# Performance work log

Hardware: AMD Instinct MI355X
Metric: run time of the kernel (lower is better)

Reference implementation:

```python
import jax, jax.numpy as jnp
import numpy as np

B, L, DM, E, N, R, S = 2, 1024, 512, 1024, 16, 32, 64
BN_SCALE = float(1.0 / np.sqrt(1.0 + 1e-5))  # eval-mode BatchNorm1d with default running stats


def _ssm(x, Wx, bx, Wdt, bdt, A_log, D):
    # x: [B,L,E] -> Mamba selective scan output [B,L,E]
    dbc = x @ Wx.T + bx                                   # [B,L,R+2N]
    delta = jax.nn.softplus(dbc[..., :R] @ Wdt.T + bdt)   # [B,L,E]
    Bm = dbc[..., R:R + N]                                # [B,L,N]
    Cm = dbc[..., R + N:]                                 # [B,L,N]
    A = -jnp.exp(A_log)                                   # [E,N]
    dA = jnp.exp(delta[..., None] * A)                    # [B,L,E,N]
    dBx = delta[..., None] * Bm[:, :, None, :] * x[..., None]

    def comb(c1, c2):
        a1, b1 = c1
        a2, b2 = c2
        return a1 * a2, b1 * a2 + b2

    _, h = jax.lax.associative_scan(comb, (dA, dBx), axis=1)  # [B,L,E,N]
    return jnp.einsum('blen,bln->ble', h, Cm) + D * x


def _gmask_idx(length, batch):
    ref = (length + 1) // 2
    idx = jnp.arange(length, dtype=jnp.float32)
    sigma = jnp.abs(idx - ref).mean()
    w = jnp.exp(-0.5 * (idx - ref) ** 2 / sigma ** 2)
    w = w / w.sum()
    return jnp.broadcast_to(w, (batch, length))


def _gmask_vec(seq):
    length = seq.shape[1]
    ref = seq[:, (length + 1) // 2, :]
    d = jnp.linalg.norm(seq - ref[:, None, :], axis=2)    # [B,L]
    sigma = d.mean(axis=1, keepdims=True)
    w = jnp.exp(-0.5 * (d / sigma) ** 2)
    return w / w.sum(axis=1, keepdims=True)


def _spatial_attn(x, w, b):
    # x: [B,L,C]; SpatialAttention: returns weighted map in [B,C,L] layout
    xt = jnp.swapaxes(x, 1, 2)                            # [B,C,L]
    fmap = (w[0] * xt.max(axis=1) + w[1] * xt.mean(axis=1) + b) * BN_SCALE
    wmap = jax.nn.sigmoid(jax.nn.relu(fmap))[:, None, :]  # [B,1,L]
    return xt * wmap                                      # [B,C,L]


def _forward(x, W_in_x, b_in_x, W_in_z, b_in_z, convf_w, convf_b, convb_w, convb_b,
             Wx_f, bx_f, Wdt_f, bdt_f, A_log_f, D_f,
             Wx_b, bx_b, Wdt_b, bdt_b, A_log_b, D_b,
             W_cat, b_cat, sa_w, sa_b, wA_f, wV_f,
             W_proj, b_proj, W_Bi, b_Bi, tf_w, tf_b, W_out, b_out):
    b_, l_, _ = x.shape
    xi = x @ W_in_x.T + b_in_x                            # [B,L,E]
    z = x @ W_in_z.T + b_in_z                             # [B,L,E]
    # depthwise conv1d with kernel_size=1 == per-channel affine
    x_f = jax.nn.silu(xi * convf_w + convf_b)
    x_b = jax.nn.silu(jnp.flip(xi, axis=1) * convb_w + convb_b)
    y_f = jnp.tanh(_ssm(x_f, Wx_f, bx_f, Wdt_f, bdt_f, A_log_f, D_f))
    y_b = jnp.tanh(_ssm(x_b, Wx_b, bx_b, Wdt_b, bdt_b, A_log_b, D_b))
    gi = _gmask_idx(l_, b_)
    mf = jax.nn.softmax(gi * _gmask_vec(y_f), axis=1)
    mb = jax.nn.softmax(gi * _gmask_vec(y_b), axis=1)
    y_cat = jnp.concatenate([y_f * mf[..., None],
                             y_b * jnp.flip(mb[..., None], axis=1)], axis=-1)
    y = y_cat @ W_cat.T + b_cat                           # [B,L,E]
    m = jax.nn.softmax(gi * _gmask_vec(y_cat), axis=1)
    y = y * m[..., None]
    yw = _spatial_attn(y, sa_w, sa_b)                     # [B,E,L]
    y = jnp.swapaxes(yw, 1, 2)                            # [B,L,E]
    # STL tokenizer (forward direction weights)
    Aw = jax.nn.softmax(jnp.swapaxes(y @ wA_f.T, 1, 2), axis=-1)  # [B,S,L]
    u = Aw @ (y @ wV_f)                                   # [B,S,E]
    # z branch: adaptive average pool L -> S (L % S == 0), then SiLU
    zp = jax.nn.silu(jnp.swapaxes(z, 1, 2).reshape(b_, E, S, l_ // S).mean(-1))
    zt = jnp.swapaxes(zp, 1, 2)                           # [B,S,E]
    # TokenFuser -- faithful to original's .view-based memory reinterpretation
    Y = (u.reshape(b_, E, S) @ W_proj.T + b_proj).reshape(b_, S, E)
    Bw = jax.nn.sigmoid(zt @ W_Bi.T + b_Bi)               # [B,S,S]
    BwY = Bw @ Y                                          # [B,S,E]
    xj = _spatial_attn(zt, tf_w, tf_b).reshape(b_, S, E)  # view (reshape), not transpose
    out = BwY + xj
    return jnp.tanh(out @ W_out.T + b_out)                # [B,S,DM]


def setup_inputs():
    ks = jax.random.split(jax.random.key(0), 24)
    g = lambda i, shape, s=0.02: jax.random.normal(ks[i], shape, dtype=jnp.float32) * s
    A_log = jnp.log(jnp.tile(jnp.arange(1, N + 1, dtype=jnp.float32), (E, 1)))
    return dict(
        x=jax.random.normal(ks[0], (B, L, DM), dtype=jnp.float32),
        W_in_x=g(1, (E, DM)), b_in_x=jnp.zeros((E,), jnp.float32),
        W_in_z=g(2, (E, DM)), b_in_z=jnp.zeros((E,), jnp.float32),
        convf_w=1.0 + g(3, (E,)), convf_b=jnp.zeros((E,), jnp.float32),
        convb_w=1.0 + g(4, (E,)), convb_b=jnp.zeros((E,), jnp.float32),
        Wx_f=g(5, (R + 2 * N, E)), bx_f=jnp.zeros((R + 2 * N,), jnp.float32),
        Wdt_f=g(6, (E, R)), bdt_f=jnp.full((E,), -4.0, jnp.float32),
        A_log_f=A_log, D_f=jnp.ones((E,), jnp.float32),
        Wx_b=g(7, (R + 2 * N, E)), bx_b=jnp.zeros((R + 2 * N,), jnp.float32),
        Wdt_b=g(8, (E, R)), bdt_b=jnp.full((E,), -4.0, jnp.float32),
        A_log_b=A_log, D_b=jnp.ones((E,), jnp.float32),
        W_cat=g(9, (E, 2 * E)), b_cat=jnp.zeros((E,), jnp.float32),
        sa_w=g(10, (2,), 0.5), sa_b=jnp.zeros((), jnp.float32),
        wA_f=g(11, (S, E), 0.05), wV_f=g(12, (E, E), 0.02),
        W_proj=g(13, (S, S), 0.1), b_proj=jnp.zeros((S,), jnp.float32),
        W_Bi=g(14, (S, E)), b_Bi=jnp.zeros((S,), jnp.float32),
        tf_w=g(15, (2,), 0.5), tf_b=jnp.zeros((), jnp.float32),
        W_out=g(16, (DM, E)), b_out=jnp.zeros((DM,), jnp.float32),
    )


def reference(x, W_in_x, b_in_x, W_in_z, b_in_z, convf_w, convf_b, convb_w, convb_b,
              Wx_f, bx_f, Wdt_f, bdt_f, A_log_f, D_f,
              Wx_b, bx_b, Wdt_b, bdt_b, A_log_b, D_b,
              W_cat, b_cat, sa_w, sa_b, wA_f, wV_f,
              W_proj, b_proj, W_Bi, b_Bi, tf_w, tf_b, W_out, b_out):
    return _forward(x, W_in_x, b_in_x, W_in_z, b_in_z, convf_w, convf_b, convb_w, convb_b,
                    Wx_f, bx_f, Wdt_f, bdt_f, A_log_f, D_f,
                    Wx_b, bx_b, Wdt_b, bdt_b, A_log_b, D_b,
                    W_cat, b_cat, sa_w, sa_b, wA_f, wV_f,
                    W_proj, b_proj, W_Bi, b_Bi, tf_w, tf_b, W_out, b_out)
```

## Files before the change

### kernel.cpp

```cpp
#include <hip/hip_runtime.h>
#include <math.h>

#define DEVI static __device__ __forceinline__

namespace {

constexpr float BN_SCALE_C = 0.9999950000374997f;

typedef __bf16 bf8v __attribute__((ext_vector_type(8)));
typedef float f4v __attribute__((ext_vector_type(4)));

DEVI float sigmoidf_(float x){ return 1.0f/(1.0f+expf(-x)); }
DEVI float siluf_(float x){ return x/(1.0f+expf(-x)); }
DEVI float softplusf_(float x){ return fmaxf(x,0.0f) + log1pf(expf(-fabsf(x))); }

DEVI unsigned short f2bf(float f){
  union{float f; unsigned int u;} v; v.f=f;
  unsigned int r = v.u + 0x7fffu + ((v.u>>16)&1u);
  return (unsigned short)(r>>16);
}

DEVI float bredw_sum(float v, float* sh){
  #pragma unroll
  for (int o=32;o;o>>=1) v += __shfl_xor(v, o);
  __syncthreads();
  if ((threadIdx.x&63)==0) sh[threadIdx.x>>6] = v;
  __syncthreads();
  return sh[0]+sh[1]+sh[2]+sh[3];
}
DEVI float bredw_max(float v, float* sh){
  #pragma unroll
  for (int o=32;o;o>>=1) v = fmaxf(v, __shfl_xor(v, o));
  __syncthreads();
  if ((threadIdx.x&63)==0) sh[threadIdx.x>>6] = v;
  __syncthreads();
  return fmaxf(fmaxf(sh[0],sh[1]), fmaxf(sh[2],sh[3]));
}

DEVI void gld_lds16(const unsigned short* g, unsigned short* l){
  __builtin_amdgcn_global_load_lds(
      (const __attribute__((address_space(1))) unsigned int*)(g),
      (__attribute__((address_space(3))) unsigned int*)(l), 16, 0, 0);
}

DEVI void stage_tile64(const unsigned short* __restrict__ Ak,
                       const unsigned short* __restrict__ Bk,
                       size_t lda, size_t ldb,
                       unsigned short* As, unsigned short* Bs,
                       int w, int lane)
{
  #pragma unroll
  for (int i=0;i<2;++i){
    int seg = (w<<1) + i;
    int row = (seg<<3) + (lane>>3);
    int c   = (lane & 7) ^ (row & 7);
    gld_lds16(Ak + (size_t)row*lda + (c<<3), As + (seg<<9));
    gld_lds16(Bk + (size_t)row*ldb + (c<<3), Bs + (seg<<9));
  }
}

DEVI void gemm_core(const unsigned short* __restrict__ Ag,
                    const unsigned short* __restrict__ Bg,
                    size_t lda, size_t ldb, int ksteps,
                    unsigned short* As, unsigned short* Bs, f4v (&acc)[2][2])
{
  const int tid = threadIdx.x;
  const int lane = tid & 63, w = tid >> 6;
  const int wr = w >> 1, wc = w & 1;
  const int l15 = lane & 15, l4 = lane >> 4;

  int cur = 0;
  stage_tile64(Ag, Bg, lda, ldb, As, Bs, w, lane);
  asm volatile("s_waitcnt vmcnt(0)" ::: "memory");
  __syncthreads();
  for (int ks = 0; ks < ksteps; ++ks){
    unsigned short* Asc = As + (cur<<12);
    unsigned short* Bsc = Bs + (cur<<12);
    if (ks+1 < ksteps)
      stage_tile64(Ag + (size_t)(ks+1)*64, Bg + (size_t)(ks+1)*64, lda, ldb,
                   As + ((cur^1)<<12), Bs + ((cur^1)<<12), w, lane);
    #pragma unroll
    for (int kk=0;kk<2;++kk){
      int cb = (kk<<2) + l4;
      bf8v af[2], bfv[2];
      #pragma unroll
      for (int mi=0;mi<2;++mi){
        int row = (wr<<5)+(mi<<4)+l15;
        af[mi] = *(const bf8v*)(Asc + (row<<6) + ((cb^(row&7))<<3));
      }
      #pragma unroll
      for (int ni=0;ni<2;++ni){
        int row = (wc<<5)+(ni<<4)+l15;
        bfv[ni] = *(const bf8v*)(Bsc + (row<<6) + ((cb^(row&7))<<3));
      }
      #pragma unroll
      for (int mi=0;mi<2;++mi)
        #pragma unroll
        for (int ni=0;ni<2;++ni)
          acc[mi][ni] = __builtin_amdgcn_mfma_f32_16x16x32_bf16(af[mi], bfv[ni], acc[mi][ni], 0,0,0);
    }
    asm volatile("s_waitcnt vmcnt(0)" ::: "memory");
    __syncthreads();
    cur ^= 1;
  }
}

template<int EPI>
__global__ __launch_bounds__(256) void gemm_bf16_k(
    const unsigned short* __restrict__ A, const unsigned short* __restrict__ Bt,
    const float* __restrict__ bias, void* __restrict__ Cout,
    int N, int K,
    const unsigned short* __restrict__ Bt2, const float* __restrict__ bias2, long sC,
    int mshift, long sB)
{
  __shared__ unsigned short As[8192], Bs[8192];
  float* Cf = (float*)Cout;
  if (Bt2 && blockIdx.z){ Bt = Bt2; bias = bias2; Cf += sC; }
  const int m0 = blockIdx.y<<6, n0 = blockIdx.x<<6;
  const unsigned short* Bb = Bt + (size_t)(m0>>mshift)*sB;
  f4v acc[2][2] = {};
  gemm_core(A + (size_t)m0*K, Bb + (size_t)n0*K, K, K, K>>6, As, Bs, acc);
  const int lane = threadIdx.x & 63, w = threadIdx.x >> 6;
  const int wr = w>>1, wc = w&1, l15 = lane&15, l4 = lane>>4;
  #pragma unroll
  for (int mi=0;mi<2;++mi)
    #pragma unroll
    for (int ni=0;ni<2;++ni){
      int col = n0 + (wc<<5) + (ni<<4) + l15;
      float bv = (EPI!=1 && bias) ? bias[col] : 0.f;
      #pragma unroll
      for (int r=0;r<4;++r){
        int rowg = m0 + (wr<<5) + (mi<<4) + (l4<<2) + r;
        float v = acc[mi][ni][r] + bv;
        if (EPI==1){
          ((unsigned short*)Cout)[(size_t)rowg*N + col] = f2bf(v);
        } else {
          if (EPI==2) v = tanhf(v);
          Cf[(size_t)rowg*N + col] = v;
        }
      }
    }
}

__global__ __launch_bounds__(256) void gemm_dbc_k(
    const unsigned short* __restrict__ A, const unsigned short* __restrict__ Wx_bf,
    const float* __restrict__ bx_f, const float* __restrict__ bx_b,
    float* __restrict__ dbcF)
{
  __shared__ unsigned short As[8192], Bs[8192];
  const int m0 = blockIdx.y<<6;
  const int dir = m0 >> 11;
  f4v acc[2][2] = {};
  gemm_core(A + (size_t)m0*1024, Wx_bf + (size_t)dir*65536, 1024, 1024, 16, As, Bs, acc);
  const float* bx = dir ? bx_b : bx_f;
  const int lane = threadIdx.x & 63, w = threadIdx.x >> 6;
  const int wr = w>>1, wc = w&1, l15 = lane&15, l4 = lane>>4;
  #pragma unroll
  for (int mi=0;mi<2;++mi)
    #pragma unroll
    for (int ni=0;ni<2;++ni){
      int col = (wc<<5) + (ni<<4) + l15;
      float bv = bx[col];
      #pragma unroll
      for (int r=0;r<4;++r){
        int rowg = m0 + (wr<<5) + (mi<<4) + (l4<<2) + r;
        dbcF[(size_t)rowg*64 + col] = acc[mi][ni][r] + bv;
      }
    }
}

__global__ __launch_bounds__(256) void castall_k(
    const float* __restrict__ s0, unsigned short* __restrict__ d0, int n0,
    const float* __restrict__ s1, unsigned short* __restrict__ d1, int n1,
    const float* __restrict__ s2, unsigned short* __restrict__ d2, int n2,
    const float* __restrict__ s3, unsigned short* __restrict__ d3, int n3,
    const float* __restrict__ s4, unsigned short* __restrict__ d4, int n4,
    const float* __restrict__ s5, unsigned short* __restrict__ d5, int n5,
    const float* __restrict__ s6, unsigned short* __restrict__ d6, int n6,
    const float* __restrict__ s7, unsigned short* __restrict__ d7, int n7,
    const float* __restrict__ wV, unsigned short* __restrict__ wVT,
    const float* __restrict__ Wdt_f, const float* __restrict__ Wdt_b,
    float* __restrict__ WdtT)
{
  __shared__ float tsh[32][33];
  if (blockIdx.x >= 4800){
    int tb = blockIdx.x - 4800;
    int tx = threadIdx.x & 31, ty = threadIdx.x >> 5;
    if (tb < 1024){
      int by = tb >> 5, bx = tb & 31;
      #pragma unroll
      for (int r=0;r<4;++r){
        int row = by*32 + ty + r*8;
        tsh[ty + r*8][tx] = wV[(long)row*1024 + bx*32 + tx];
      }
      __syncthreads();
      #pragma unroll
      for (int r=0;r<4;++r){
        int row = bx*32 + ty + r*8;
        wVT[(long)row*1024 + by*32 + tx] = f2bf(tsh[tx][ty + r*8]);
      }
    } else {
      int q = tb - 1024;
      int dir = q >> 5, bi = q & 31;
      const float* src = dir ? Wdt_b : Wdt_f;
      float* dst = WdtT + (dir<<15);
      #pragma unroll
      for (int r=0;r<4;++r){
        int row = bi*32 + ty + r*8;
        tsh[ty + r*8][tx] = src[(long)row*32 + tx];
      }
      __syncthreads();
      #pragma unroll
      for (int r=0;r<4;++r){
        int c = ty + r*8;
        dst[(long)c*1024 + bi*32 + tx] = tsh[tx][c];
      }
    }
    return;
  }
  int i = (blockIdx.x*256 + threadIdx.x)*4;
  const float* s; unsigned short* d;
  if (i < n0){ s = s0; d = d0; }
  else if ((i -= n0) < n1){ s = s1; d = d1; }
  else if ((i -= n1) < n2){ s = s2; d = d2; }
  else if ((i -= n2) < n3){ s = s3; d = d3; }
  else if ((i -= n3) < n4){ s = s4; d = d4; }
  else if ((i -= n4) < n5){ s = s5; d = d5; }
  else if ((i -= n5) < n6){ s = s6; d = d6; }
  else if ((i -= n6) < n7){ s = s7; d = d7; }
  else return;
  float4 v = *(const float4*)(s + i);
  union{ unsigned short u[4]; uint2 p; } o;
  o.u[0]=f2bf(v.x); o.u[1]=f2bf(v.y); o.u[2]=f2bf(v.z); o.u[3]=f2bf(v.w);
  *(uint2*)(d + i) = o.p;
}

__global__ __launch_bounds__(256) void convzt_k(const float* __restrict__ xi, const float* __restrict__ z,
    const float* __restrict__ cfw, const float* __restrict__ cfb,
    const float* __restrict__ cbw, const float* __restrict__ cbb,
    float* __restrict__ xf, float* __restrict__ xb, unsigned short* __restrict__ xfb_bf,
    float* __restrict__ ztb)
{
  int bx = blockIdx.x, t = threadIdx.x;
  if (bx < 2048){
    int base = (bx*256 + t) << 2;
    int e = base & 1023;
    int bl = base >> 10; int l = bl & 1023, b = bl >> 10;
    float4 cw = *(const float4*)(cfw + e);
    float4 cb = *(const float4*)(cfb + e);
    float4 xv = *(const float4*)(xi + base);
    float4 vf;
    vf.x = siluf_(fmaf(xv.x, cw.x, cb.x));
    vf.y = siluf_(fmaf(xv.y, cw.y, cb.y));
    vf.z = siluf_(fmaf(xv.z, cw.z, cb.z));
    vf.w = siluf_(fmaf(xv.w, cw.w, cb.w));
    *(float4*)(xf + base) = vf;
    union{unsigned short u[4]; uint2 p;} o;
    o.u[0]=f2bf(vf.x); o.u[1]=f2bf(vf.y); o.u[2]=f2bf(vf.z); o.u[3]=f2bf(vf.w);
    *(uint2*)(xfb_bf + base) = o.p;
    int jb = (((b<<10) + (1023-l))<<10) + e;
    float4 cw2 = *(const float4*)(cbw + e);
    float4 cb2 = *(const float4*)(cbb + e);
    float4 xw = *(const float4*)(xi + jb);
    float4 vb;
    vb.x = siluf_(fmaf(xw.x, cw2.x, cb2.x));
    vb.y = siluf_(fmaf(xw.y, cw2.y, cb2.y));
    vb.z = siluf_(fmaf(xw.z, cw2.z, cb2.z));
    vb.w = siluf_(fmaf(xw.w, cw2.w, cb2.w));
    *(float4*)(xb + base) = vb;
    union{unsigned short u[4]; uint2 p;} o2;
    o2.u[0]=f2bf(vb.x); o2.u[1]=f2bf(vb.y); o2.u[2]=f2bf(vb.z); o2.u[3]=f2bf(vb.w);
    *(uint2*)(xfb_bf + 2097152 + base) = o2.p;
  } else {
    int base = ((bx-2048)*256 + t) << 2;
    int e = base & 1023; int bs = base >> 10; int s = bs & 63; int b = bs >> 6;
    const float* zp = z + (((long)((b<<10)+(s<<4)))<<10) + e;
    float4 sm = {0.f,0.f,0.f,0.f};
    #pragma unroll
    for (int j=0;j<16;++j){
      float4 v = *(const float4*)(zp + ((long)j<<10));
      sm.x += v.x; sm.y += v.y; sm.z += v.z; sm.w += v.w;
    }
    float4 o;
    o.x = siluf_(sm.x*(1.f/16.f)); o.y = siluf_(sm.y*(1.f/16.f));
    o.z = siluf_(sm.z*(1.f/16.f)); o.w = siluf_(sm.w*(1.f/16.f));
    *(float4*)(ztb + base) = o;
  }
}

__global__ __launch_bounds__(256) void dbcdelta_k(
    const float* __restrict__ dbcF, const float* __restrict__ WdtT,
    const float* __restrict__ bdt_f, const float* __restrict__ bdt_b,
    float* __restrict__ delta)
{
  __shared__ float sdbc[8][64];
  const int t = threadIdx.x;
  const int r0 = blockIdx.x * 8;
  const int dir = r0 >> 11;
  const float* bdt = dir ? bdt_b : bdt_f;
  const float* WT  = WdtT + (dir<<15);
  for (int idx=t; idx<512; idx+=256){
    int r = idx>>6, c = idx&63;
    sdbc[r][c] = dbcF[(long)(r0+r)*64 + c];
  }
  __syncthreads();
  const int c0 = t << 2;
  float4 bv = *(const float4*)(bdt + c0);
  float4 acc[8];
  #pragma unroll
  for (int r=0;r<8;++r) acc[r] = bv;
  #pragma unroll
  for (int k=0;k<32;++k){
    float4 w = *(const float4*)(WT + (k<<10) + c0);
    #pragma unroll
    for (int r=0;r<8;++r){
      float a = sdbc[r][k];
      acc[r].x = fmaf(a, w.x, acc[r].x);
      acc[r].y = fmaf(a, w.y, acc[r].y);
      acc[r].z = fmaf(a, w.z, acc[r].z);
      acc[r].w = fmaf(a, w.w, acc[r].w);
    }
  }
  #pragma unroll
  for (int r=0;r<8;++r){
    float4 o;
    o.x = softplusf_(acc[r].x); o.y = softplusf_(acc[r].y);
    o.z = softplusf_(acc[r].z); o.w = softplusf_(acc[r].w);
    *(float4*)(delta + (long)(r0+r)*1024 + c0) = o;
  }
}

__global__ __launch_bounds__(256) void ssm_chunk_k(
    const float* __restrict__ xs0, const float* __restrict__ dl0,
    const float* __restrict__ dbc0, const float* __restrict__ A_log_f,
    const float* __restrict__ A_log_b,
    float* __restrict__ pA0, float* __restrict__ hend0)
{
  const int dir = blockIdx.y;
  const float* xs   = xs0  + (size_t)dir*2097152;
  const float* delta= dl0  + (size_t)dir*2097152;
  const float* dbc  = dbc0 + (size_t)dir*131072;
  const float* A_log= dir ? A_log_b : A_log_f;
  float* pA   = pA0   + (size_t)dir*1048576;
  float* hend = hend0 + (size_t)dir*1048576;

  __shared__ float sB[32][16];
  int g = blockIdx.x*256 + threadIdx.x;
  int e = g & 1023;
  int bc = g >> 10;
  int c = bc & 31, b = bc >> 5;
  for (int i=threadIdx.x; i<512; i+=256){
    int l=i>>4, n=i&15;
    sB[l][n] = dbc[(((b<<10) + (c<<5) + l)<<6) + 32 + n];
  }
  __syncthreads();
  float An[16];
  #pragma unroll
  for (int n=0;n<16;++n) An[n] = -__expf(A_log[(e<<4)+n]);
  float h[16], p[16];
  #pragma unroll
  for (int n=0;n<16;++n){ h[n]=0.0f; p[n]=1.0f; }
  long base = ((long)((b<<10) + (c<<5)))*1024 + e;
  for (int l=0;l<32;++l){
    float dl = delta[base + ((long)l<<10)];
    float xv = xs[base + ((long)l<<10)];
    float dx = dl*xv;
    #pragma unroll
    for (int n=0;n<16;++n){
      float a = __expf(dl*An[n]);
      h[n] = fmaf(a, h[n], dx*sB[l][n]);
      p[n] *= a;
    }
  }
  long ob = ((long)((b<<5)+c)<<4)*1024 + e;
  #pragma unroll
  for (int n=0;n<16;++n){ pA[ob + ((long)n<<10)] = p[n]; hend[ob + ((long)n<<10)] = h[n]; }
}

__global__ __launch_bounds__(256) void ssm_carry_k(
    const float* __restrict__ pA, const float* __restrict__ hend, float* __restrict__ Hc)
{
  int i = blockIdx.x*256 + threadIdx.x;
  int e = i & 1023, n = (i>>10)&15, b = (i>>14)&1, dir = (i>>15)&1;
  const float* pAd = pA   + (size_t)dir*1048576;
  const float* hd  = hend + (size_t)dir*1048576;
  float* Hd        = Hc   + (size_t)dir*1048576;
  float H = 0.f;
  long base = ((long)(b*512 + n))*1024 + e;
  for (int c=0;c<32;++c){
    long a = base + (long)c*16384;
    Hd[a] = H;
    H = fmaf(pAd[a], H, hd[a]);
  }
}

__global__ __launch_bounds__(256) void ssm_out_k(
    const float* __restrict__ xs0, const float* __restrict__ dl0,
    const float* __restrict__ dbc0, const float* __restrict__ A_log_f,
    const float* __restrict__ A_log_b, const float* __restrict__ Hc0,
    const float* __restrict__ D_f, const float* __restrict__ D_b,
    float* __restrict__ y0)
{
  const int dir = blockIdx.y;
  const float* xs   = xs0  + (size_t)dir*2097152;
  const float* delta= dl0  + (size_t)dir*2097152;
  const float* dbc  = dbc0 + (size_t)dir*131072;
  const float* A_log= dir ? A_log_b : A_log_f;
  const float* Hc   = Hc0 + (size_t)dir*1048576;
  const float* D    = dir ? D_b : D_f;
  float* y          = y0 + (size_t)dir*2097152;

  __shared__ float sB[32][16], sC[32][16];
  int g = blockIdx.x*256+threadIdx.x;
  int e = g & 1023;
  int bc = g >> 10;
  int c = bc & 31, b = bc >> 5;
  for (int i=threadIdx.x;i<512;i+=256){
    int l=i>>4, n=i&15;
    int base = ((b<<10)+(c<<5)+l)<<6;
    sB[l][n] = dbc[base+32+n];
    sC[l][n] = dbc[base+48+n];
  }
  __syncthreads();
  float An[16], h[16];
  long ib = ((long)((b<<5)+c)<<4)*1024 + e;
  #pragma unroll
  for(int n=0;n<16;++n){ An[n] = -__expf(A_log[(e<<4)+n]); h[n]=Hc[ib+((long)n<<10)]; }
  float Dv = D[e];
  long base = ((long)((b<<10)+(c<<5)))*1024 + e;
  for (int l=0;l<32;++l){
    float dl = delta[base+((long)l<<10)];
    float xv = xs[base+((long)l<<10)];
    float dx = dl*xv;
    float acc = Dv*xv;
    #pragma unroll
    for(int n=0;n<16;++n){
      float a = __expf(dl*An[n]);
      h[n] = fmaf(a,h[n],dx*sB[l][n]);
      acc = fmaf(h[n], sC[l][n], acc);
    }
    y[base+((long)l<<10)] = tanhf(acc);
  }
}

__global__ __launch_bounds__(256) void stats_k(const float* __restrict__ y,
    float* __restrict__ nrm, float* __restrict__ dotv)
{
  __shared__ float sh[4];
  int row = blockIdx.x;
  int rowref = (row & ~1023) + 512;
  const float4* rp  = (const float4*)(y + (long)row*1024);
  const float4* rf  = (const float4*)(y + (long)rowref*1024);
  float4 a = rp[threadIdx.x], r = rf[threadIdx.x];
  float sn = a.x*a.x + a.y*a.y + a.z*a.z + a.w*a.w;
  float sd = a.x*r.x + a.y*r.y + a.z*r.z + a.w*r.w;
  sn = bredw_sum(sn, sh);
  sd = bredw_sum(sd, sh);
  if (threadIdx.x==0){ nrm[row] = sn; dotv[row] = sd; }
}

DEVI void softmask(const float (&d)[4], const float (&gi)[4], float gsum,
                   float* sh, float (&m)[4])
{
  float s = d[0]+d[1]+d[2]+d[3];
  float sig = bredw_sum(s, sh) * (1.0f/1024.0f);
  float inv = 1.0f/sig;
  float w[4]; s = 0.f;
  #pragma unroll
  for (int i=0;i<4;++i){ float r = d[i]*inv; w[i] = __expf(-0.5f*r*r); s += w[i]; }
  float wsm = bredw_sum(s, sh);
  float sc = 1.0f/(wsm*gsum);
  float tv[4]; float mx = -1e30f;
  #pragma unroll
  for (int i=0;i<4;++i){ tv[i] = gi[i]*w[i]*sc; mx = fmaxf(mx, tv[i]); }
  mx = bredw_max(mx, sh);
  s = 0.f;
  #pragma unroll
  for (int i=0;i<4;++i){ tv[i] = __expf(tv[i]-mx); s += tv[i]; }
  float es = bredw_sum(s, sh);
  float ie = 1.0f/es;
  #pragma unroll
  for (int i=0;i<4;++i) m[i] = tv[i]*ie;
}

__global__ __launch_bounds__(256) void mask2_k(
    const float* __restrict__ nrm, const float* __restrict__ dotv,
    float* __restrict__ mfG, float* __restrict__ mbG, float* __restrict__ mvG)
{
  __shared__ float mfs[1024], mbs[1024], sh[4];
  const int b = blockIdx.x, t = threadIdx.x;
  const float nf512 = nrm[(b<<10)+512];
  const float nb512 = nrm[2048+(b<<10)+512];
  float gi[4], nf[4], pf[4], nb[4], pb[4];
  float gs = 0.f;
  #pragma unroll
  for (int i=0;i<4;++i){
    int l = t + (i<<8);
    float q = (float)(l-512) * (1.0f/256.0f);
    gi[i] = __expf(-0.5f*q*q); gs += gi[i];
    nf[i] = nrm[(b<<10)+l];      pf[i] = dotv[(b<<10)+l];
    nb[i] = nrm[2048+(b<<10)+l]; pb[i] = dotv[2048+(b<<10)+l];
  }
  float gsum = bredw_sum(gs, sh);
  float mf[4], mb[4], d[4];
  #pragma unroll
  for (int i=0;i<4;++i) d[i] = sqrtf(fmaxf(nf[i] - 2.f*pf[i] + nf512, 0.f));
  softmask(d, gi, gsum, sh, mf);
  #pragma unroll
  for (int i=0;i<4;++i) d[i] = sqrtf(fmaxf(nb[i] - 2.f*pb[i] + nb512, 0.f));
  softmask(d, gi, gsum, sh, mb);
  #pragma unroll
  for (int i=0;i<4;++i){
    int l = t + (i<<8);
    mfs[l] = mf[i]; mbs[l] = mb[i];
    mfG[(b<<10)+l] = mf[i]; mbG[(b<<10)+l] = mb[i];
  }
  __syncthreads();
  const float mf512 = mfs[512], mb511 = mbs[511];
  #pragma unroll
  for (int i=0;i<4;++i){
    int l = t + (i<<8);
    float mbf = mbs[1023-l];
    float dc2 = mf[i]*mf[i]*nf[i] - 2.f*mf[i]*mf512*pf[i] + mf512*mf512*nf512
              + mbf*mbf*nb[i]     - 2.f*mbf*mb511*pb[i]   + mb511*mb511*nb512;
    d[i] = sqrtf(fmaxf(dc2, 0.f));
  }
  float mv[4];
  softmask(d, gi, gsum, sh, mv);
  #pragma unroll
  for (int i=0;i<4;++i) mvG[(b<<10)+t+(i<<8)] = mv[i];
}

__global__ __launch_bounds__(256) void ycat_k(const float* __restrict__ yf, const float* __restrict__ yb,
    const float* __restrict__ mf, const float* __restrict__ mb, unsigned short* __restrict__ yc)
{
  int base = (blockIdx.x*256 + threadIdx.x) << 2;
  int e = base & 1023; int bl = base >> 10; int l = bl & 1023, b = bl >> 10;
  float mfv = mf[bl];
  float mbv = mb[(b<<10) + (1023-l)];
  float4 vf = *(const float4*)(yf + base);
  float4 vb = *(const float4*)(yb + base);
  long r = (long)bl*2048;
  union{unsigned short u[4]; uint2 p;} o;
  o.u[0]=f2bf(vf.x*mfv); o.u[1]=f2bf(vf.y*mfv); o.u[2]=f2bf(vf.z*mfv); o.u[3]=f2bf(vf.w*mfv);
  *(uint2*)(yc + r + e) = o.p;
  union{unsigned short u[4]; uint2 p;} o2;
  o2.u[0]=f2bf(vb.x*mbv); o2.u[1]=f2bf(vb.y*mbv); o2.u[2]=f2bf(vb.z*mbv); o2.u[3]=f2bf(vb.w*mbv);
  *(uint2*)(yc + r + 1024 + e) = o2.p;
}

__global__ __launch_bounds__(256) void rowscale_k(const float* __restrict__ y, const float* __restrict__ m,
    const float* __restrict__ sw, const float* __restrict__ sb, unsigned short* __restrict__ yo)
{
  __shared__ float sh[4];
  int row = blockIdx.x;
  float mv = m[row];
  float4 v = ((const float4*)(y + (long)row*1024))[threadIdx.x];
  v.x *= mv; v.y *= mv; v.z *= mv; v.w *= mv;
  float mx = fmaxf(fmaxf(v.x,v.y), fmaxf(v.z,v.w));
  float sm = v.x+v.y+v.z+v.w;
  float rmax = bredw_max(mx, sh);
  float rsum = bredw_sum(sm, sh);
  float fmap = (sw[0]*rmax + sw[1]*(rsum*(1.0f/1024.0f)) + sb[0])*BN_SCALE_C;
  float sc = sigmoidf_(fmaxf(fmap, 0.0f));
  union{unsigned short u[4]; uint2 p;} o;
  o.u[0]=f2bf(v.x*sc); o.u[1]=f2bf(v.y*sc); o.u[2]=f2bf(v.z*sc); o.u[3]=f2bf(v.w*sc);
  *(uint2*)(yo + (long)row*1024 + (threadIdx.x<<2)) = o.p;
}

__global__ __launch_bounds__(256) void awsmT_k(const float* __restrict__ yA,
    unsigned short* __restrict__ Aw,
    const unsigned short* __restrict__ src, unsigned short* __restrict__ dst)
{
  __shared__ float sh[4];
  __shared__ unsigned short tsh[32][33];
  if (blockIdx.x < 128){
    int bs = blockIdx.x; int b = bs >> 6, s = bs & 63;
    float v[4]; float mx=-1e30f;
    #pragma unroll
    for(int i=0;i<4;++i){
      int l = threadIdx.x+(i<<8);
      v[i] = yA[(long)((b<<10)+l)*64 + s];
      mx = fmaxf(mx, v[i]);
    }
    mx = bredw_max(mx, sh);
    float sm=0.0f;
    #pragma unroll
    for(int i=0;i<4;++i){ v[i]=__expf(v[i]-mx); sm+=v[i]; }
    sm = bredw_sum(sm, sh);
    float inv = 1.0f/sm;
    #pragma unroll
    for(int i=0;i<4;++i){ int l=threadIdx.x+(i<<8); Aw[(((b<<6)+s)<<10)+l] = f2bf(v[i]*inv); }
  } else {
    int tb = blockIdx.x - 128;
    size_t bo = (size_t)(tb>>10) << 20;
    int rem = tb & 1023;
    int by = rem >> 5, bx = rem & 31;
    int tx = threadIdx.x & 31, ty = threadIdx.x >> 5;
    #pragma unroll
    for (int r=0;r<4;++r){
      int row = by*32 + ty + r*8;
      tsh[ty + r*8][tx] = src[bo + (long)row*1024 + bx*32 + tx];
    }
    __syncthreads();
    #pragma unroll
    for (int r=0;r<4;++r){
      int row = bx*32 + ty + r*8;
      dst[bo + (long)row*1024 + by*32 + tx] = tsh[tx][ty + r*8];
    }
  }
}

__global__ __launch_bounds__(256) void upbw_k(const float* __restrict__ u2f,
    const float* __restrict__ W_proj, const float* __restrict__ b_proj,
    const float* __restrict__ zt, const float* __restrict__ W_Bi,
    const float* __restrict__ b_Bi, const float* __restrict__ tw,
    const float* __restrict__ tb,
    float* __restrict__ Yp, float* __restrict__ Bw, float* __restrict__ gz)
{
  __shared__ float a[1024];
  __shared__ float sh[4];
  const int t = threadIdx.x;
  if (blockIdx.x < 256){
    const int r0 = blockIdx.x*8;
    for (int idx=t; idx<512; idx+=256){
      int r = idx>>6, sp = idx&63;
      a[idx] = u2f[(long)(r0+r)*64 + sp];
    }
    __syncthreads();
    int r = t >> 5, c = t & 31;
    const float* ar = a + (r<<6);
    float acc1 = b_proj[c], acc2 = b_proj[c+32];
    for (int sp=0; sp<64; ++sp){
      float av = ar[sp];
      acc1 = fmaf(av, W_proj[c*64+sp], acc1);
      acc2 = fmaf(av, W_proj[(c+32)*64+sp], acc2);
    }
    long row = r0 + r;
    Yp[row*64 + c] = acc1;
    Yp[row*64 + c + 32] = acc2;
  } else {
    const int row = blockIdx.x - 256;
    float4 zv = ((const float4*)(zt + (long)row*1024))[t];
    *(float4*)(a + (t<<2)) = zv;
    float mx = fmaxf(fmaxf(zv.x,zv.y), fmaxf(zv.z,zv.w));
    float sm = zv.x+zv.y+zv.z+zv.w;
    mx = bredw_max(mx, sh);
    sm = bredw_sum(sm, sh);
    if (t==0){
      float f = (tw[0]*mx + tw[1]*(sm*(1.0f/1024.0f)) + tb[0])*BN_SCALE_C;
      gz[row] = sigmoidf_(fmaxf(f,0.0f));
    }
    __syncthreads();
    int col = t >> 2, q = t & 3;
    const float4* wp = (const float4*)(W_Bi + (long)col*1024 + q*256);
    const float4* zp = (const float4*)(a + q*256);
    float acc = 0.f;
    for (int i=0;i<64;++i){
      float4 w = wp[i], zc = zp[i];
      acc += w.x*zc.x + w.y*zc.y + w.z*zc.z + w.w*zc.w;
    }
    acc += __shfl_xor(acc, 1);
    acc += __shfl_xor(acc, 2);
    if (q==0) Bw[(long)row*64 + col] = sigmoidf_(acc + b_Bi[col]);
  }
}

__global__ __launch_bounds__(256) void o_k(const float* __restrict__ Bw,
    const float* __restrict__ Yp, const float* __restrict__ zt,
    const float* __restrict__ gz, unsigned short* __restrict__ O_bf)
{
  __shared__ float bwrow[64];
  const int t = threadIdx.x;
  const int bs = blockIdx.x; const int b = bs >> 6, s = bs & 63;
  if (t < 64) bwrow[t] = Bw[(long)bs*64 + t];
  __syncthreads();
  const int e0 = t << 2;
  const float* yb = Yp + (long)b*65536 + e0;
  float4 acc = {0.f,0.f,0.f,0.f};
  for (int s2=0; s2<64; ++s2){
    float f = bwrow[s2];
    float4 y = *(const float4*)(yb + ((long)s2<<10));
    acc.x = fmaf(f,y.x,acc.x); acc.y = fmaf(f,y.y,acc.y);
    acc.z = fmaf(f,y.z,acc.z); acc.w = fmaf(f,y.w,acc.w);
  }
  int ez = (s<<4) + (e0>>6);
  float o4[4] = {acc.x, acc.y, acc.z, acc.w};
  union{unsigned short u[4]; uint2 p;} o;
  #pragma unroll
  for (int k=0;k<4;++k){
    int sz = (e0&63) + k;
    float xj = zt[(((long)((b<<6)+sz))<<10) + ez] * gz[(b<<6)+sz];
    o.u[k] = f2bf(o4[k] + xj);
  }
  *(uint2*)(O_bf + (long)bs*1024 + e0) = o.p;
}

}

extern "C" void kernel_launch(void* const* d_in, const int* in_sizes, int n_in,
                              void* d_out, int out_size, void* d_ws, size_t ws_size,
                              hipStream_t stream)
{
  (void)in_sizes; (void)n_in; (void)out_size; (void)ws_size;
  const float* x      = (const float*)d_in[0];
  const float* W_in_x = (const float*)d_in[1];
  const float* b_in_x = (const float*)d_in[2];
  const float* W_in_z = (const float*)d_in[3];
  const float* b_in_z = (const float*)d_in[4];
  const float* cfw    = (const float*)d_in[5];
  const float* cfb    = (const float*)d_in[6];
  const float* cbw    = (const float*)d_in[7];
  const float* cbb    = (const float*)d_in[8];
  const float* Wx_f   = (const float*)d_in[9];
  const float* bx_f   = (const float*)d_in[10];
  const float* Wdt_f  = (const float*)d_in[11];
  const float* bdt_f  = (const float*)d_in[12];
  const float* A_log_f= (const float*)d_in[13];
  const float* D_f    = (const float*)d_in[14];
  const float* Wx_b   = (const float*)d_in[15];
  const float* bx_b   = (const float*)d_in[16];
  const float* Wdt_b  = (const float*)d_in[17];
  const float* bdt_b  = (const float*)d_in[18];
  const float* A_log_b= (const float*)d_in[19];
  const float* D_b    = (const float*)d_in[20];
  const float* W_cat  = (const float*)d_in[21];
  const float* b_cat  = (const float*)d_in[22];
  const float* sa_w   = (const float*)d_in[23];
  const float* sa_b   = (const float*)d_in[24];
  const float* wA_f   = (const float*)d_in[25];
  const float* wV_f   = (const float*)d_in[26];
  const float* W_proj = (const float*)d_in[27];
  const float* b_proj = (const float*)d_in[28];
  const float* W_Bi   = (const float*)d_in[29];
  const float* b_Bi   = (const float*)d_in[30];
  const float* tf_w   = (const float*)d_in[31];
  const float* tf_b   = (const float*)d_in[32];
  const float* W_out  = (const float*)d_in[33];
  const float* b_out  = (const float*)d_in[34];
  float* out = (float*)d_out;
  float* ws  = (float*)d_ws;

  const size_t M1 = 1u<<20;
  float* xi = ws;
  float* pA = ws;
  unsigned short* ycat_bf = (unsigned short*)ws;
  float* z = ws + 2*M1;
  float* hend = ws + 2*M1;
  float* ybufF = ws + 2*M1;
  float* xf = ws + 4*M1;
  unsigned short* ybuf_bf = (unsigned short*)(ws + 4*M1);
  float* xb = ws + 6*M1;
  unsigned short* ybufT_bf = (unsigned short*)(ws + 6*M1);
  float* yf = ws + 8*M1;
  float* yb = ws + 10*M1;
  float* u2f = ws + 10*M1;
  unsigned short* xfxb_bf = (unsigned short*)(ws + 12*M1);
  float* deltaF = ws + 12*M1;
  unsigned short* x_bf = (unsigned short*)(ws + 17*M1);
  float* Hc = ws + 16*M1;
  float* dbcF = ws + 18*M1;
  size_t woff = 18*M1 + 262144;
  unsigned short* Winx_bf = (unsigned short*)(ws + woff); woff += 262144;
  unsigned short* Winz_bf = (unsigned short*)(ws + woff); woff += 262144;
  unsigned short* Wcat_bf = (unsigned short*)(ws + woff); woff += M1;
  unsigned short* wVT_bf  = (unsigned short*)(ws + woff); woff += 524288;
  unsigned short* wA_bf   = (unsigned short*)(ws + woff); woff += 32768;
  unsigned short* Wx_bf   = (unsigned short*)(ws + woff); woff += 65536;
  unsigned short* Wout_bf = (unsigned short*)(ws + woff); woff += 262144;
  float* WdtT = ws + woff; woff += 65536;
  float* ztb  = ws + woff; woff += 131072;
  float* nrm  = ws + woff; woff += 4096;
  float* dotv = ws + woff; woff += 4096;
  float* mfG  = ws + woff; woff += 2048;
  float* mbG  = ws + woff; woff += 2048;
  float* mvG  = ws + woff; woff += 2048;
  float* gz   = ws + woff; woff += 256;
  float* yA   = ws + woff; woff += 131072;
  unsigned short* Aw_bf = (unsigned short*)(ws + woff); woff += 65536;
  unsigned short* uR_bf = (unsigned short*)(ws + woff); woff += 65536;
  float* Yp   = ws + woff; woff += 131072;
  float* Bw   = ws + woff; woff += 8192;
  unsigned short* O_bf = (unsigned short*)(ws + woff); woff += 65536;

  dim3 blk(256);

  castall_k<<<5888,blk,0,stream>>>(x, x_bf, 1048576,
                                   W_in_x, Winx_bf, 524288,
                                   W_in_z, Winz_bf, 524288,
                                   W_cat, Wcat_bf, 2097152,
                                   wA_f, wA_bf, 65536,
                                   Wx_f, Wx_bf, 65536,
                                   Wx_b, Wx_bf + 65536, 65536,
                                   W_out, Wout_bf, 524288,
                                   wV_f, wVT_bf, Wdt_f, Wdt_b, WdtT);

  gemm_bf16_k<0><<<dim3(16,32,2),blk,0,stream>>>(x_bf, Winx_bf, b_in_x, xi, 1024, 512,
                                                 Winz_bf, b_in_z, (long)(2*M1), 31, 0);
  convzt_k<<<2176,blk,0,stream>>>(xi, z, cfw,cfb,cbw,cbb, xf, xb, xfxb_bf, ztb);

  gemm_dbc_k<<<dim3(1,64),blk,0,stream>>>(xfxb_bf, Wx_bf, bx_f, bx_b, dbcF);
  dbcdelta_k<<<512,blk,0,stream>>>(dbcF, WdtT, bdt_f, bdt_b, deltaF);

  ssm_chunk_k<<<dim3(256,2),blk,0,stream>>>(xf, deltaF, dbcF, A_log_f, A_log_b, pA, hend);
  ssm_carry_k<<<256,blk,0,stream>>>(pA, hend, Hc);
  ssm_out_k<<<dim3(256,2),blk,0,stream>>>(xf, deltaF, dbcF, A_log_f, A_log_b, Hc, D_f, D_b, yf);

  stats_k<<<4096,blk,0,stream>>>(yf, nrm, dotv);
  mask2_k<<<2,blk,0,stream>>>(nrm, dotv, mfG, mbG, mvG);
  ycat_k<<<2048,blk,0,stream>>>(yf, yb, mfG, mbG, ycat_bf);

  gemm_bf16_k<0><<<dim3(16,32,1),blk,0,stream>>>(ycat_bf, Wcat_bf, b_cat, ybufF, 1024, 2048,
                                                 nullptr, nullptr, 0, 31, 0);
  rowscale_k<<<2048,blk,0,stream>>>(ybufF, mvG, sa_w, sa_b, ybuf_bf);

  gemm_bf16_k<0><<<dim3(1,32,1),blk,0,stream>>>(ybuf_bf, wA_bf, nullptr, yA, 64, 1024,
                                                nullptr, nullptr, 0, 31, 0);
  awsmT_k<<<2176,blk,0,stream>>>(yA, Aw_bf, ybuf_bf, ybufT_bf);
  gemm_bf16_k<1><<<dim3(16,2,1),blk,0,stream>>>(Aw_bf, ybufT_bf, nullptr, uR_bf, 1024, 1024,
                                                nullptr, nullptr, 0, 6, (long)M1);
  gemm_bf16_k<0><<<dim3(16,2,1),blk,0,stream>>>(uR_bf, wVT_bf, nullptr, u2f, 1024, 1024,
                                                nullptr, nullptr, 0, 31, 0);

  upbw_k<<<384,blk,0,stream>>>(u2f, W_proj, b_proj, ztb, W_Bi, b_Bi, tf_w, tf_b, Yp, Bw, gz);
  o_k<<<128,blk,0,stream>>>(Bw, Yp, ztb, gz, O_bf);

  gemm_bf16_k<2><<<dim3(8,2,1),blk,0,stream>>>(O_bf, Wout_bf, b_out, out, 512, 1024,
                                               nullptr, nullptr, 0, 31, 0);
}
```

Baseline: 229.4 us.

## Fuse delta projection into SSM scans and add split-K GEMM for small grids

Removes the separate dbcdelta kernel and its full delta buffer: both SSM scan kernels now recompute delta per element from the dbc row (staged in shared memory) and per-thread Wdt registers, then apply softplus. A new split-K GEMM kernel, which gives each warp a quarter of K and reduces through LDS, replaces the generic GEMM for the low-block-count launches (dbc, wA, attention, wV and output projections). softplus also switches to fast __expf. The aim is less global traffic, one fewer launch, and more parallelism in the tiny-grid GEMMs, at the cost of computing delta twice and using more registers and LDS.

Result: faster. 217.7 us (-5.1%).

```diff
diff --git a/kernel.cpp b/kernel.cpp
--- a/kernel.cpp
+++ b/kernel.cpp
@@ -12,7 +12,7 @@
 
 DEVI float sigmoidf_(float x){ return 1.0f/(1.0f+expf(-x)); }
 DEVI float siluf_(float x){ return x/(1.0f+expf(-x)); }
-DEVI float softplusf_(float x){ return fmaxf(x,0.0f) + log1pf(expf(-fabsf(x))); }
+DEVI float softplusf_(float x){ return fmaxf(x,0.0f) + log1pf(__expf(-fabsf(x))); }
 
 DEVI unsigned short f2bf(float f){
   union{float f; unsigned int u;} v; v.f=f;
@@ -110,16 +110,14 @@
     const unsigned short* __restrict__ A, const unsigned short* __restrict__ Bt,
     const float* __restrict__ bias, void* __restrict__ Cout,
     int N, int K,
-    const unsigned short* __restrict__ Bt2, const float* __restrict__ bias2, long sC,
-    int mshift, long sB)
+    const unsigned short* __restrict__ Bt2, const float* __restrict__ bias2, long sC)
 {
   __shared__ unsigned short As[8192], Bs[8192];
   float* Cf = (float*)Cout;
   if (Bt2 && blockIdx.z){ Bt = Bt2; bias = bias2; Cf += sC; }
   const int m0 = blockIdx.y<<6, n0 = blockIdx.x<<6;
-  const unsigned short* Bb = Bt + (size_t)(m0>>mshift)*sB;
   f4v acc[2][2] = {};
-  gemm_core(A + (size_t)m0*K, Bb + (size_t)n0*K, K, K, K>>6, As, Bs, acc);
+  gemm_core(A + (size_t)m0*K, Bt + (size_t)n0*K, K, K, K>>6, As, Bs, acc);
   const int lane = threadIdx.x & 63, w = threadIdx.x >> 6;
   const int wr = w>>1, wc = w&1, l15 = lane&15, l4 = lane>>4;
   #pragma unroll
@@ -127,46 +125,123 @@
     #pragma unroll
     for (int ni=0;ni<2;++ni){
       int col = n0 + (wc<<5) + (ni<<4) + l15;
-      float bv = (EPI!=1 && bias) ? bias[col] : 0.f;
+      float bv = bias ? bias[col] : 0.f;
       #pragma unroll
       for (int r=0;r<4;++r){
         int rowg = m0 + (wr<<5) + (mi<<4) + (l4<<2) + r;
-        float v = acc[mi][ni][r] + bv;
-        if (EPI==1){
-          ((unsigned short*)Cout)[(size_t)rowg*N + col] = f2bf(v);
-        } else {
-          if (EPI==2) v = tanhf(v);
-          Cf[(size_t)rowg*N + col] = v;
+        Cf[(size_t)rowg*N + col] = acc[mi][ni][r] + bv;
+      }
+    }
+}
+
+template<int EPI>
+__global__ __launch_bounds__(256) void gemm_small_k(
+    const unsigned short* __restrict__ A, const unsigned short* __restrict__ Bt,
+    const float* __restrict__ b0, const float* __restrict__ b1,
+    void* __restrict__ Cout, int N, int K, int mshift, long sB)
+{
+  __shared__ unsigned char smem[65536];
+  unsigned short* AsAll = (unsigned short*)smem;
+  unsigned short* BsAll = (unsigned short*)(smem + 32768);
+  float* Lc = (float*)smem;
+
+  const int tid = threadIdx.x;
+  const int lane = tid & 63, w = tid >> 6;
+  const int m0 = blockIdx.y<<6, n0 = blockIdx.x<<6;
+  const unsigned short* Ab = A + (size_t)m0*K;
+  const unsigned short* Bb = Bt + (size_t)(m0>>mshift)*sB + (size_t)n0*K;
+  unsigned short* Asw = AsAll + (w<<12);
+  unsigned short* Bsw = BsAll + (w<<12);
+  const int kpw = K >> 2;
+  const int nst = kpw >> 6;
+  const int l15 = lane & 15, l4 = lane >> 4;
+  const int srow8 = lane >> 3, sc = lane & 7;
+
+  f4v acc[4][4] = {};
+  for (int ks = 0; ks < nst; ++ks){
+    const int kbase = w*kpw + (ks<<6);
+    #pragma unroll
+    for (int seg=0; seg<8; ++seg){
+      int row = (seg<<3) + srow8;
+      int c = sc ^ (row & 7);
+      gld_lds16(Ab + (size_t)row*K + kbase + (c<<3), Asw + (seg<<9));
+      gld_lds16(Bb + (size_t)row*K + kbase + (c<<3), Bsw + (seg<<9));
+    }
+    asm volatile("s_waitcnt vmcnt(0)" ::: "memory");
+    #pragma unroll
+    for (int kk=0; kk<2; ++kk){
+      int cb = (kk<<2) + l4;
+      bf8v af[4], bfv[4];
+      #pragma unroll
+      for (int mi=0;mi<4;++mi){
+        int row = (mi<<4) + l15;
+        af[mi] = *(const bf8v*)(Asw + (row<<6) + ((cb^(row&7))<<3));
+      }
+      #pragma unroll
+      for (int ni=0;ni<4;++ni){
+        int row = (ni<<4) + l15;
+        bfv[ni] = *(const bf8v*)(Bsw + (row<<6) + ((cb^(row&7))<<3));
+      }
+      #pragma unroll
+      for (int mi=0;mi<4;++mi)
+        #pragma unroll
+        for (int ni=0;ni<4;++ni)
+          acc[mi][ni] = __builtin_amdgcn_mfma_f32_16x16x32_bf16(af[mi], bfv[ni], acc[mi][ni], 0,0,0);
+    }
+    __builtin_amdgcn_sched_barrier(0);
+  }
+  __syncthreads();
+  #pragma unroll
+  for (int mi=0;mi<4;++mi)
+    #pragma unroll
+    for (int ni=0;ni<4;++ni){
+      int col = (ni<<4) + l15;
+      #pragma unroll
+      for (int r=0;r<4;++r){
+        int row = (mi<<4) + (l4<<2) + r;
+        Lc[(w<<12) + (row<<6) + col] = acc[mi][ni][r];
+      }
+    }
+  __syncthreads();
+  {
+    const int basei = tid << 4;
+    const int row = basei >> 6, colb = basei & 63;
+    float vals[16];
+    #pragma unroll
+    for (int q=0;q<4;++q){
+      float4 a0 = *(const float4*)(Lc + basei + (q<<2));
+      float4 a1 = *(const float4*)(Lc + 4096 + basei + (q<<2));
+      float4 a2 = *(const float4*)(Lc + 8192 + basei + (q<<2));
+      float4 a3 = *(const float4*)(Lc + 12288 + basei + (q<<2));
+      vals[(q<<2)+0] = a0.x+a1.x+a2.x+a3.x;
+      vals[(q<<2)+1] = a0.y+a1.y+a2.y+a3.y;
+      vals[(q<<2)+2] = a0.z+a1.z+a2.z+a3.z;
+      vals[(q<<2)+3] = a0.w+a1.w+a2.w+a3.w;
+    }
+    if (EPI==1){
+      unsigned short* Cb = (unsigned short*)Cout + (size_t)(m0+row)*N + n0 + colb;
+      union{unsigned short u[16]; uint4 q[2];} o;
+      #pragma unroll
+      for (int j=0;j<16;++j) o.u[j] = f2bf(vals[j]);
+      *(uint4*)(Cb) = o.q[0];
+      *(uint4*)(Cb+8) = o.q[1];
+    } else {
+      const float* bias = (b1 && (m0>>mshift)) ? b1 : b0;
+      float* Cb = (float*)Cout + (size_t)(m0+row)*N + n0 + colb;
+      #pragma unroll
+      for (int q=0;q<4;++q){
+        float4 v;
+        float* vp = &v.x;
+        #pragma unroll
+        for (int j=0;j<4;++j){
+          float t = vals[(q<<2)+j] + (bias ? bias[n0+colb+(q<<2)+j] : 0.f);
+          if (EPI==2) t = tanhf(t);
+          vp[j] = t;
         }
-      }
-    }
-}
-
-__global__ __launch_bounds__(256) void gemm_dbc_k(
-    const unsigned short* __restrict__ A, const unsigned short* __restrict__ Wx_bf,
-    const float* __restrict__ bx_f, const float* __restrict__ bx_b,
-    float* __restrict__ dbcF)
-{
-  __shared__ unsigned short As[8192], Bs[8192];
-  const int m0 = blockIdx.y<<6;
-  const int dir = m0 >> 11;
-  f4v acc[2][2] = {};
-  gemm_core(A + (size_t)m0*1024, Wx_bf + (size_t)dir*65536, 1024, 1024, 16, As, Bs, acc);
-  const float* bx = dir ? bx_b : bx_f;
-  const int lane = threadIdx.x & 63, w = threadIdx.x >> 6;
-  const int wr = w>>1, wc = w&1, l15 = lane&15, l4 = lane>>4;
-  #pragma unroll
-  for (int mi=0;mi<2;++mi)
-    #pragma unroll
-    for (int ni=0;ni<2;++ni){
-      int col = (wc<<5) + (ni<<4) + l15;
-      float bv = bx[col];
-      #pragma unroll
-      for (int r=0;r<4;++r){
-        int rowg = m0 + (wr<<5) + (mi<<4) + (l4<<2) + r;
-        dbcF[(size_t)rowg*64 + col] = acc[mi][ni][r] + bv;
-      }
-    }
+        *(float4*)(Cb + (q<<2)) = v;
+      }
+    }
+  }
 }
 
 __global__ __launch_bounds__(256) void castall_k(
@@ -288,63 +363,22 @@
   }
 }
 
-__global__ __launch_bounds__(256) void dbcdelta_k(
-    const float* __restrict__ dbcF, const float* __restrict__ WdtT,
+__global__ __launch_bounds__(256) void ssm_chunk_k(
+    const float* __restrict__ xs0, const float* __restrict__ dbc0,
+    const float* __restrict__ A_log_f, const float* __restrict__ A_log_b,
+    const float* __restrict__ WdtT,
     const float* __restrict__ bdt_f, const float* __restrict__ bdt_b,
-    float* __restrict__ delta)
-{
-  __shared__ float sdbc[8][64];
-  const int t = threadIdx.x;
-  const int r0 = blockIdx.x * 8;
-  const int dir = r0 >> 11;
-  const float* bdt = dir ? bdt_b : bdt_f;
-  const float* WT  = WdtT + (dir<<15);
-  for (int idx=t; idx<512; idx+=256){
-    int r = idx>>6, c = idx&63;
-    sdbc[r][c] = dbcF[(long)(r0+r)*64 + c];
-  }
-  __syncthreads();
-  const int c0 = t << 2;
-  float4 bv = *(const float4*)(bdt + c0);
-  float4 acc[8];
-  #pragma unroll
-  for (int r=0;r<8;++r) acc[r] = bv;
-  #pragma unroll
-  for (int k=0;k<32;++k){
-    float4 w = *(const float4*)(WT + (k<<10) + c0);
-    #pragma unroll
-    for (int r=0;r<8;++r){
-      float a = sdbc[r][k];
-      acc[r].x = fmaf(a, w.x, acc[r].x);
-      acc[r].y = fmaf(a, w.y, acc[r].y);
-      acc[r].z = fmaf(a, w.z, acc[r].z);
-      acc[r].w = fmaf(a, w.w, acc[r].w);
-    }
-  }
-  #pragma unroll
-  for (int r=0;r<8;++r){
-    float4 o;
-    o.x = softplusf_(acc[r].x); o.y = softplusf_(acc[r].y);
-    o.z = softplusf_(acc[r].z); o.w = softplusf_(acc[r].w);
-    *(float4*)(delta + (long)(r0+r)*1024 + c0) = o;
-  }
-}
-
-__global__ __launch_bounds__(256) void ssm_chunk_k(
-    const float* __restrict__ xs0, const float* __restrict__ dl0,
-    const float* __restrict__ dbc0, const float* __restrict__ A_log_f,
-    const float* __restrict__ A_log_b,
     float* __restrict__ pA0, float* __restrict__ hend0)
 {
   const int dir = blockIdx.y;
   const float* xs   = xs0  + (size_t)dir*2097152;
-  const float* delta= dl0  + (size_t)dir*2097152;
   const float* dbc  = dbc0 + (size_t)dir*131072;
   const float* A_log= dir ? A_log_b : A_log_f;
   float* pA   = pA0   + (size_t)dir*1048576;
   float* hend = hend0 + (size_t)dir*1048576;
 
   __shared__ float sB[32][16];
+  __shared__ float sD[32][32];
   int g = blockIdx.x*256 + threadIdx.x;
   int e = g & 1023;
   int bc = g >> 10;
@@ -353,7 +387,18 @@
     int l=i>>4, n=i&15;
     sB[l][n] = dbc[(((b<<10) + (c<<5) + l)<<6) + 32 + n];
   }
-  __syncthreads();
+  for (int i=threadIdx.x; i<1024; i+=256){
+    int l=i>>5, k=i&31;
+    sD[l][k] = dbc[(((b<<10) + (c<<5) + l)<<6) + k];
+  }
+  __syncthreads();
+  float wdt[32];
+  {
+    const float* WT = WdtT + (dir<<15) + e;
+    #pragma unroll
+    for (int k=0;k<32;++k) wdt[k] = WT[(size_t)k<<10];
+  }
+  const float bde = (dir ? bdt_b : bdt_f)[e];
   float An[16];
   #pragma unroll
   for (int n=0;n<16;++n) An[n] = -__expf(A_log[(e<<4)+n]);
@@ -362,7 +407,10 @@
   for (int n=0;n<16;++n){ h[n]=0.0f; p[n]=1.0f; }
   long base = ((long)((b<<10) + (c<<5)))*1024 + e;
   for (int l=0;l<32;++l){
-    float dl = delta[base + ((long)l<<10)];
+    float accd = bde;
+    #pragma unroll
+    for (int k=0;k<32;++k) accd = fmaf(sD[l][k], wdt[k], accd);
+    float dl = softplusf_(accd);
     float xv = xs[base + ((long)l<<10)];
     float dx = dl*xv;
     #pragma unroll
@@ -395,15 +443,16 @@
 }
 
 __global__ __launch_bounds__(256) void ssm_out_k(
-    const float* __restrict__ xs0, const float* __restrict__ dl0,
-    const float* __restrict__ dbc0, const float* __restrict__ A_log_f,
-    const float* __restrict__ A_log_b, const float* __restrict__ Hc0,
+    const float* __restrict__ xs0, const float* __restrict__ dbc0,
+    const float* __restrict__ A_log_f, const float* __restrict__ A_log_b,
+    const float* __restrict__ WdtT,
+    const float* __restrict__ bdt_f, const float* __restrict__ bdt_b,
+    const float* __restrict__ Hc0,
     const float* __restrict__ D_f, const float* __restrict__ D_b,
     float* __restrict__ y0)
 {
   const int dir = blockIdx.y;
   const float* xs   = xs0  + (size_t)dir*2097152;
-  const float* delta= dl0  + (size_t)dir*2097152;
   const float* dbc  = dbc0 + (size_t)dir*131072;
   const float* A_log= dir ? A_log_b : A_log_f;
   const float* Hc   = Hc0 + (size_t)dir*1048576;
@@ -411,6 +460,7 @@
   float* y          = y0 + (size_t)dir*2097152;
 
   __shared__ float sB[32][16], sC[32][16];
+  __shared__ float sD[32][32];
   int g = blockIdx.x*256+threadIdx.x;
   int e = g & 1023;
   int bc = g >> 10;
@@ -421,7 +471,18 @@
     sB[l][n] = dbc[base+32+n];
     sC[l][n] = dbc[base+48+n];
   }
-  __syncthreads();
+  for (int i=threadIdx.x; i<1024; i+=256){
+    int l=i>>5, k=i&31;
+    sD[l][k] = dbc[(((b<<10) + (c<<5) + l)<<6) + k];
+  }
+  __syncthreads();
+  float wdt[32];
+  {
+    const float* WT = WdtT + (dir<<15) + e;
+    #pragma unroll
+    for (int k=0;k<32;++k) wdt[k] = WT[(size_t)k<<10];
+  }
+  const float bde = (dir ? bdt_b : bdt_f)[e];
   float An[16], h[16];
   long ib = ((long)((b<<5)+c)<<4)*1024 + e;
   #pragma unroll
@@ -429,7 +490,10 @@
   float Dv = D[e];
   long base = ((long)((b<<10)+(c<<5)))*1024 + e;
   for (int l=0;l<32;++l){
-    float dl = delta[base+((long)l<<10)];
+    float accd = bde;
+    #pragma unroll
+    for (int k=0;k<32;++k) accd = fmaf(sD[l][k], wdt[k], accd);
+    float dl = softplusf_(accd);
     float xv = xs[base+((long)l<<10)];
     float dx = dl*xv;
     float acc = Dv*xv;
@@ -756,7 +820,6 @@
   float* yb = ws + 10*M1;
   float* u2f = ws + 10*M1;
   unsigned short* xfxb_bf = (unsigned short*)(ws + 12*M1);
-  float* deltaF = ws + 12*M1;
   unsigned short* x_bf = (unsigned short*)(ws + 17*M1);
   float* Hc = ws + 16*M1;
   float* dbcF = ws + 18*M1;
@@ -796,35 +859,37 @@
                                    wV_f, wVT_bf, Wdt_f, Wdt_b, WdtT);
 
   gemm_bf16_k<0><<<dim3(16,32,2),blk,0,stream>>>(x_bf, Winx_bf, b_in_x, xi, 1024, 512,
-                                                 Winz_bf, b_in_z, (long)(2*M1), 31, 0);
+                                                 Winz_bf, b_in_z, (long)(2*M1));
   convzt_k<<<2176,blk,0,stream>>>(xi, z, cfw,cfb,cbw,cbb, xf, xb, xfxb_bf, ztb);
 
-  gemm_dbc_k<<<dim3(1,64),blk,0,stream>>>(xfxb_bf, Wx_bf, bx_f, bx_b, dbcF);
-  dbcdelta_k<<<512,blk,0,stream>>>(dbcF, WdtT, bdt_f, bdt_b, deltaF);
-
-  ssm_chunk_k<<<dim3(256,2),blk,0,stream>>>(xf, deltaF, dbcF, A_log_f, A_log_b, pA, hend);
+  gemm_small_k<0><<<dim3(1,64),blk,0,stream>>>(xfxb_bf, Wx_bf, bx_f, bx_b, dbcF,
+                                               64, 1024, 11, 65536);
+
+  ssm_chunk_k<<<dim3(256,2),blk,0,stream>>>(xf, dbcF, A_log_f, A_log_b,
+                                            WdtT, bdt_f, bdt_b, pA, hend);
   ssm_carry_k<<<256,blk,0,stream>>>(pA, hend, Hc);
-  ssm_out_k<<<dim3(256,2),blk,0,stream>>>(xf, deltaF, dbcF, A_log_f, A_log_b, Hc, D_f, D_b, yf);
+  ssm_out_k<<<dim3(256,2),blk,0,stream>>>(xf, dbcF, A_log_f, A_log_b,
+                                          WdtT, bdt_f, bdt_b, Hc, D_f, D_b, yf);
 
   stats_k<<<4096,blk,0,stream>>>(yf, nrm, dotv);
   mask2_k<<<2,blk,0,stream>>>(nrm, dotv, mfG, mbG, mvG);
   ycat_k<<<2048,blk,0,stream>>>(yf, yb, mfG, mbG, ycat_bf);
 
   gemm_bf16_k<0><<<dim3(16,32,1),blk,0,stream>>>(ycat_bf, Wcat_bf, b_cat, ybufF, 1024, 2048,
-                                                 nullptr, nullptr, 0, 31, 0);
+                                                 nullptr, nullptr, 0);
   rowscale_k<<<2048,blk,0,stream>>>(ybufF, mvG, sa_w, sa_b, ybuf_bf);
 
-  gemm_bf16_k<0><<<dim3(1,32,1),blk,0,stream>>>(ybuf_bf, wA_bf, nullptr, yA, 64, 1024,
-                                                nullptr, nullptr, 0, 31, 0);
+  gemm_small_k<0><<<dim3(1,32),blk,0,stream>>>(ybuf_bf, wA_bf, nullptr, nullptr, yA,
+                                               64, 1024, 31, 0);
   awsmT_k<<<2176,blk,0,stream>>>(yA, Aw_bf, ybuf_bf, ybufT_bf);
-  gemm_bf16_k<1><<<dim3(16,2,1),blk,0,stream>>>(Aw_bf, ybufT_bf, nullptr, uR_bf, 1024, 1024,
-                                                nullptr, nullptr, 0, 6, (long)M1);
-  gemm_bf16_k<0><<<dim3(16,2,1),blk,0,stream>>>(uR_bf, wVT_bf, nullptr, u2f, 1024, 1024,
-                                                nullptr, nullptr, 0, 31, 0);
+  gemm_small_k<1><<<dim3(16,2),blk,0,stream>>>(Aw_bf, ybufT_bf, nullptr, nullptr, uR_bf,
+                                               1024, 1024, 6, (long)M1);
+  gemm_small_k<0><<<dim3(16,2),blk,0,stream>>>(uR_bf, wVT_bf, nullptr, nullptr, u2f,
+                                               1024, 1024, 31, 0);
 
   upbw_k<<<384,blk,0,stream>>>(u2f, W_proj, b_proj, ztb, W_Bi, b_Bi, tf_w, tf_b, Yp, Bw, gz);
   o_k<<<128,blk,0,stream>>>(Bw, Yp, ztb, gz, O_bf);
 
-  gemm_bf16_k<2><<<dim3(8,2,1),blk,0,stream>>>(O_bf, Wout_bf, b_out, out, 512, 1024,
-                                               nullptr, nullptr, 0, 31, 0);
-}
+  gemm_small_k<2><<<dim3(8,2),blk,0,stream>>>(O_bf, Wout_bf, b_out, nullptr, out,
+                                              512, 1024, 31, 0);
+}
```
